# Kernel tuning notes

Hardware: AMD Instinct MI355X
Metric: run time of the kernel (lower is better)

Reference implementation:

```python
import jax, jax.numpy as jnp
import numpy as np

B, S, D, H = 2, 2048, 1024, 16
DH = D // H  # 64


def _rotate_half(t):
    x1, x2 = jnp.split(t, 2, axis=-1)
    return jnp.concatenate([-x2, x1], axis=-1)


def setup_inputs() -> dict:
    key = jax.random.key(0)
    ks = jax.random.split(key, 11)
    x = jax.random.normal(ks[0], (B, S, D), dtype=jnp.float32)
    mask = jax.random.randint(ks[1], (B, S), 0, 2, dtype=jnp.int32)
    scale = 0.02
    wq = jax.random.normal(ks[2], (D, D), dtype=jnp.float32) * scale
    bq = jnp.zeros((D,), dtype=jnp.float32)
    wk = jax.random.normal(ks[3], (D, D), dtype=jnp.float32) * scale
    bk = jnp.zeros((D,), dtype=jnp.float32)
    wv = jax.random.normal(ks[4], (D, D), dtype=jnp.float32) * scale
    bv = jnp.zeros((D,), dtype=jnp.float32)
    wo = jax.random.normal(ks[5], (D, D), dtype=jnp.float32) * scale
    bo = jnp.zeros((D,), dtype=jnp.float32)
    return {"x": x, "mask": mask, "wq": wq, "bq": bq, "wk": wk, "bk": bk,
            "wv": wv, "bv": bv, "wo": wo, "bo": bo}


def reference(x, mask, wq, bq, wk, bk, wv, bv, wo, bo):
    b, s, d = x.shape
    # QKV projections, split heads -> [B, H, S, DH]
    q = (x @ wq + bq).reshape(b, s, H, DH).transpose(0, 2, 1, 3)
    k = (x @ wk + bk).reshape(b, s, H, DH).transpose(0, 2, 1, 3)
    v = (x @ wv + bv).reshape(b, s, H, DH).transpose(0, 2, 1, 3)
    # RoPE exactly as in source: repeat(cos,2) paired with half-split rotate
    pos = jnp.arange(s, dtype=jnp.float32)
    inv_freq = 1.0 / (10000.0 ** (jnp.arange(0, DH, 2, dtype=jnp.float32) / DH))
    angle = pos[:, None] * inv_freq[None, :]            # [S, DH/2]
    cos = jnp.repeat(jnp.cos(angle), 2, axis=-1)[None, None]  # [1,1,S,DH]
    sin = jnp.repeat(jnp.sin(angle), 2, axis=-1)[None, None]
    q = q * cos + _rotate_half(q) * sin
    k = k * cos + _rotate_half(k) * sin
    # scaled dot-product attention with additive mask
    logits = jnp.einsum('bhqd,bhkd->bhqk', q, k) / jnp.sqrt(jnp.float32(DH))
    m = mask.astype(jnp.float32)[:, None, None, :]      # [B,1,1,S]
    logits = logits + m * (-1e9)
    attn = jax.nn.softmax(logits, axis=-1)
    out = jnp.einsum('bhqk,bhkd->bhqd', attn, v)
    out = out.transpose(0, 2, 1, 3).reshape(b, s, d)
    return out @ wo + bo
```

## Files before the change

### kernel.cpp

```cpp
#include <hip/hip_runtime.h>
#include <math.h>

#define BB 2
#define SS 2048
#define DD 1024
#define HH 16

typedef unsigned short u16;
using bf16x8 = __attribute__((ext_vector_type(8))) short;
using f32x4  = __attribute__((ext_vector_type(4))) float;


__device__ __forceinline__ u16 f2bf(float f) {
    unsigned u = __float_as_uint(f);
    unsigned r = u + 0x7fffu + ((u >> 16) & 1u);
    return (u16)(r >> 16);
}

__device__ __forceinline__ void gload_lds16(const void* g, const void* l) {
    __builtin_amdgcn_global_load_lds(
        (const __attribute__((address_space(1))) unsigned int*)(unsigned long long)g,
        (__attribute__((address_space(3))) unsigned int*)(unsigned int)(unsigned long long)l,
        16, 0, 0);
}

__global__ void rope_table(float* __restrict__ cost, float* __restrict__ sint) {
    int idx = blockIdx.x * 256 + threadIdx.x;
    int pos = idx >> 5;
    int j   = idx & 31;
    double inv = pow(10000.0, -(double)j / 32.0);
    double ang = (double)pos * inv;
    cost[idx] = (float)cos(ang);
    sint[idx] = (float)sin(ang);
}

__global__ void cvt_x(const float* __restrict__ x, u16* __restrict__ xb) {
    int i = (blockIdx.x * 256 + threadIdx.x) * 4;
    float4 v = *(const float4*)(x + i);
    ushort4 o;
    o.x = f2bf(v.x); o.y = f2bf(v.y); o.z = f2bf(v.z); o.w = f2bf(v.w);
    *(ushort4*)(xb + i) = o;
}

__global__ void transpose_w(const float* __restrict__ w0, const float* __restrict__ w1,
                            const float* __restrict__ w2, const float* __restrict__ w3,
                            u16* __restrict__ o0, u16* __restrict__ o1,
                            u16* __restrict__ o2, u16* __restrict__ o3) {
    const float* in = (blockIdx.z == 0) ? w0 : (blockIdx.z == 1) ? w1 : (blockIdx.z == 2) ? w2 : w3;
    u16* out        = (blockIdx.z == 0) ? o0 : (blockIdx.z == 1) ? o1 : (blockIdx.z == 2) ? o2 : o3;
    __shared__ float t[32][33];
    int n = blockIdx.x * 32 + threadIdx.x;
    for (int i = threadIdx.y; i < 32; i += 8)
        t[i][threadIdx.x] = in[(size_t)(blockIdx.y * 32 + i) * 1024 + n];
    __syncthreads();
    int k = blockIdx.y * 32 + threadIdx.x;
    for (int i = threadIdx.y; i < 32; i += 8)
        out[(size_t)(blockIdx.x * 32 + i) * 1024 + k] = f2bf(t[threadIdx.x][i]);
}

__global__ __launch_bounds__(256)
void qkv_gemm(const u16* __restrict__ xb,
              const u16* __restrict__ wtq, const u16* __restrict__ wtk, const u16* __restrict__ wtv,
              const float* __restrict__ bq, const float* __restrict__ bk, const float* __restrict__ bv,
              const float* __restrict__ cost, const float* __restrict__ sint,
              u16* __restrict__ qo, u16* __restrict__ ko, u16* __restrict__ vo)
{
    __shared__ u16 Al[128 * 32];
    __shared__ u16 Bl[128 * 32];

    int bx = blockIdx.x;
    int which = bx >> 3;
    int n0 = (bx & 7) << 7;
    int m0 = blockIdx.y << 7;
    const u16*  wt    = (which == 0) ? wtq : (which == 1) ? wtk : wtv;
    const float* bias = (which == 0) ? bq  : (which == 1) ? bk  : bv;

    int t = threadIdx.x;
    int wid = t >> 6, lane = t & 63;
    int wr = wid >> 1, wc = wid & 1;
    int fr = lane & 15, fq = lane >> 4;

    f32x4 acc[4][4];
    #pragma unroll
    for (int m = 0; m < 4; ++m)
        #pragma unroll
        for (int n = 0; n < 4; ++n)
            #pragma unroll
            for (int r = 0; r < 4; ++r) acc[m][n][r] = 0.f;

    int srow = (lane >> 2);
    int skof = (lane & 3) << 3;

    for (int k0 = 0; k0 < 1024; k0 += 32) {
        __syncthreads();
        #pragma unroll
        for (int c = 0; c < 2; ++c) {
            int chunk = wid * 2 + c;
            int row = (chunk << 4) + srow;
            gload_lds16(xb + (size_t)(m0 + row) * 1024 + k0 + skof, &Al[chunk << 9]);
            gload_lds16(wt + (size_t)(n0 + row) * 1024 + k0 + skof, &Bl[chunk << 9]);
        }
        __syncthreads();

        bf16x8 af[4], bf[4];
        #pragma unroll
        for (int m = 0; m < 4; ++m)
            af[m] = *(const bf16x8*)&Al[((wr << 6) + (m << 4) + fr) * 32 + (fq << 3)];
        #pragma unroll
        for (int n = 0; n < 4; ++n)
            bf[n] = *(const bf16x8*)&Bl[((wc << 6) + (n << 4) + fr) * 32 + (fq << 3)];
        #pragma unroll
        for (int m = 0; m < 4; ++m)
            #pragma unroll
            for (int n = 0; n < 4; ++n)
                acc[m][n] = __builtin_amdgcn_mfma_f32_16x16x32_bf16(af[m], bf[n], acc[m][n], 0, 0, 0);
    }

    if (which < 2) {
        u16* outp = (which == 0) ? qo : ko;
        const float qs = (which == 0) ? 0.125f : 1.0f;
        #pragma unroll
        for (int n = 0; n < 2; ++n) {
            int col = n0 + (wc << 6) + (n << 4) + fr;
            int h = col >> 6;
            int d = col & 63;
            float b1 = bias[col], b2 = bias[col + 32];
            int a1 = d >> 1;
            #pragma unroll
            for (int mm = 0; mm < 4; ++mm) {
                #pragma unroll
                for (int j = 0; j < 4; ++j) {
                    int mi = m0 + (wr << 6) + (mm << 4) + (fq << 2) + j;
                    int bi = mi >> 11, s = mi & 2047;
                    float c1 = cost[s * 32 + a1],      s1 = sint[s * 32 + a1];
                    float c2 = cost[s * 32 + a1 + 16], s2 = sint[s * 32 + a1 + 16];
                    float x1 = acc[mm][n][j]     + b1;
                    float x2 = acc[mm][n + 2][j] + b2;
                    size_t base = ((size_t)(bi * HH + h) * SS + s) << 6;
                    outp[base + d]      = f2bf((x1 * c1 - x2 * s1) * qs);
                    outp[base + d + 32] = f2bf((x2 * c2 + x1 * s2) * qs);
                }
            }
        }
    } else {
        #pragma unroll
        for (int n = 0; n < 4; ++n) {
            int col = n0 + (wc << 6) + (n << 4) + fr;
            int h = col >> 6, d = col & 63;
            float bb = bias[col];
            #pragma unroll
            for (int mm = 0; mm < 4; ++mm) {
                #pragma unroll
                for (int j = 0; j < 4; ++j) {
                    int mi = m0 + (wr << 6) + (mm << 4) + (fq << 2) + j;
                    int bi = mi >> 11, s = mi & 2047;
                    vo[((((size_t)(bi * HH + h)) << 6) + d) * SS + s] = f2bf(acc[mm][n][j] + bb);
                }
            }
        }
    }
}

__global__ __launch_bounds__(256, 4)
void attn(const u16* __restrict__ qb, const u16* __restrict__ kb, const u16* __restrict__ vt,
          const int* __restrict__ mask, u16* __restrict__ preb)
{
    __shared__ u16 Kl[2][4096];
    __shared__ u16 Vl[2][4096];
    __shared__ u16 Pl[4][1024];

    const int qb0 = blockIdx.x << 6;
    const int bh  = blockIdx.y;
    const int b   = bh >> 4;
    const int t   = threadIdx.x;
    const int w   = t >> 6;
    const int lane = t & 63;
    const int fr  = lane & 15;
    const int fq  = lane >> 4;
    const int swz = (fr & 7) << 4;

    const char* kbase = (const char*)(kb + ((size_t)bh << 17));
    const char* vbase = (const char*)(vt + ((size_t)bh << 17));
    const int* maskp  = mask + (b << 11);

    const int sbo = ((t & 7) << 4) ^ (((t >> 3) & 7) << 4);

    const int qrow = qb0 + (w << 4) + fr;
    const u16* qp = qb + (((size_t)bh << 11) + qrow) * 64 + (fq << 3);
    bf16x8 qf0 = *(const bf16x8*)qp;
    bf16x8 qf1 = *(const bf16x8*)(qp + 32);

    f32x4 o[4];
    #pragma unroll
    for (int n = 0; n < 4; ++n)
        #pragma unroll
        for (int r = 0; r < 4; ++r) o[n][r] = 0.f;
    float mrun = -INFINITY, lrun = 0.f;

    auto STAGE = [&](int buf, int kt) {
        #pragma unroll
        for (int c = 0; c < 2; ++c) {
            int row = (c << 5) + (t >> 3);
            gload_lds16(kbase + ((size_t)(kt << 6) + row) * 128 + sbo,
                        (const char*)&Kl[buf][0] + (c << 12) + t * 16);
            gload_lds16(vbase + (size_t)row * 4096 + (kt << 7) + sbo,
                        (const char*)&Vl[buf][0] + (c << 12) + t * 16);
        }
    };

    STAGE(0, 0);
    __syncthreads();

    for (int kt = 0; kt < 32; ++kt) {
        const int cur = kt & 1;

        float mb[16];
        #pragma unroll
        for (int g = 0; g < 4; ++g)
            #pragma unroll
            for (int j = 0; j < 4; ++j)
                mb[(g << 2) + j] = -1e9f * (float)maskp[(kt << 6) + (g << 4) + (fq << 2) + j];

        if (kt < 31) STAGE(cur ^ 1, kt + 1);

        f32x4 sv[4];
        #pragma unroll
        for (int g = 0; g < 4; ++g)
            #pragma unroll
            for (int r = 0; r < 4; ++r) sv[g][r] = 0.f;

        const char* Kb = (const char*)&Kl[cur][0];
        #pragma unroll
        for (int g = 0; g < 4; ++g) {
            int row = (g << 4) + fr;
            bf16x8 kf0 = *(const bf16x8*)(Kb + row * 128 + ((fq << 4) ^ swz));
            bf16x8 kf1 = *(const bf16x8*)(Kb + row * 128 + (((fq << 4) + 64) ^ swz));
            sv[g] = __builtin_amdgcn_mfma_f32_16x16x32_bf16(kf0, qf0, sv[g], 0, 0, 0);
            sv[g] = __builtin_amdgcn_mfma_f32_16x16x32_bf16(kf1, qf1, sv[g], 0, 0, 0);
        }

        float tm = -INFINITY;
        #pragma unroll
        for (int g = 0; g < 4; ++g)
            #pragma unroll
            for (int j = 0; j < 4; ++j) {
                sv[g][j] += mb[(g << 2) + j];
                tm = fmaxf(tm, sv[g][j]);
            }
        tm = fmaxf(tm, __shfl_xor(tm, 16));
        tm = fmaxf(tm, __shfl_xor(tm, 32));
        float newm = fmaxf(mrun, tm);
        float scale = __expf(mrun - newm);
        float ps = 0.f;
        #pragma unroll
        for (int g = 0; g < 4; ++g) {
            float p0 = __expf(sv[g][0] - newm);
            float p1 = __expf(sv[g][1] - newm);
            float p2 = __expf(sv[g][2] - newm);
            float p3 = __expf(sv[g][3] - newm);
            ps += (p0 + p1) + (p2 + p3);
            ushort4 pw;
            pw.x = f2bf(p0); pw.y = f2bf(p1); pw.z = f2bf(p2); pw.w = f2bf(p3);
            *(ushort4*)((char*)&Pl[w][0] + fr * 128 + (((g << 5) + (fq << 3)) ^ swz)) = pw;
        }
        ps += __shfl_xor(ps, 16);
        ps += __shfl_xor(ps, 32);
        lrun = lrun * scale + ps;
        mrun = newm;

        #pragma unroll
        for (int j = 0; j < 4; ++j) {
            float sj = __shfl(scale, (lane & 48) + (fq << 2) + j);
            #pragma unroll
            for (int n = 0; n < 4; ++n) o[n][j] *= sj;
        }

        #pragma unroll
        for (int kk = 0; kk < 2; ++kk) {
            bf16x8 pa = *(const bf16x8*)((const char*)&Pl[w][0] + fr * 128 + (((fq << 4) + (kk << 6)) ^ swz));
            #pragma unroll
            for (int n = 0; n < 4; ++n) {
                int row = (n << 4) + fr;
                bf16x8 vf = *(const bf16x8*)((const char*)&Vl[cur][0] + row * 128 + (((fq << 4) + (kk << 6)) ^ swz));
                o[n] = __builtin_amdgcn_mfma_f32_16x16x32_bf16(pa, vf, o[n], 0, 0, 0);
            }
        }
        __syncthreads();
    }

    #pragma unroll
    for (int j = 0; j < 4; ++j) {
        float lj = __shfl(lrun, (lane & 48) + (fq << 2) + j);
        float inv = 1.0f / lj;
        int qr = qb0 + (w << 4) + (fq << 2) + j;
        u16* op = preb + ((size_t)((b << 11) + qr) << 10) + ((bh & 15) << 6) + fr;
        #pragma unroll
        for (int n = 0; n < 4; ++n)
            op[n << 4] = f2bf(o[n][j] * inv);
    }
}

__global__ __launch_bounds__(256)
void out_gemm(const u16* __restrict__ pre, const u16* __restrict__ wto,
              const float* __restrict__ bo, float* __restrict__ outp)
{
    __shared__ u16 Al[128 * 32];
    __shared__ u16 Bl[128 * 32];

    int n0 = blockIdx.x << 7;
    int m0 = blockIdx.y << 7;

    int t = threadIdx.x;
    int wid = t >> 6, lane = t & 63;
    int wr = wid >> 1, wc = wid & 1;
    int fr = lane & 15, fq = lane >> 4;

    f32x4 acc[4][4];
    #pragma unroll
    for (int m = 0; m < 4; ++m)
        #pragma unroll
        for (int n = 0; n < 4; ++n)
            #pragma unroll
            for (int r = 0; r < 4; ++r) acc[m][n][r] = 0.f;

    int srow = (lane >> 2);
    int skof = (lane & 3) << 3;

    for (int k0 = 0; k0 < 1024; k0 += 32) {
        __syncthreads();
        #pragma unroll
        for (int c = 0; c < 2; ++c) {
            int chunk = wid * 2 + c;
            int row = (chunk << 4) + srow;
            gload_lds16(pre + (size_t)(m0 + row) * 1024 + k0 + skof, &Al[chunk << 9]);
            gload_lds16(wto + (size_t)(n0 + row) * 1024 + k0 + skof, &Bl[chunk << 9]);
        }
        __syncthreads();

        bf16x8 af[4], bf[4];
        #pragma unroll
        for (int m = 0; m < 4; ++m)
            af[m] = *(const bf16x8*)&Al[((wr << 6) + (m << 4) + fr) * 32 + (fq << 3)];
        #pragma unroll
        for (int n = 0; n < 4; ++n)
            bf[n] = *(const bf16x8*)&Bl[((wc << 6) + (n << 4) + fr) * 32 + (fq << 3)];
        #pragma unroll
        for (int m = 0; m < 4; ++m)
            #pragma unroll
            for (int n = 0; n < 4; ++n)
                acc[m][n] = __builtin_amdgcn_mfma_f32_16x16x32_bf16(af[m], bf[n], acc[m][n], 0, 0, 0);
    }

    #pragma unroll
    for (int n = 0; n < 4; ++n) {
        int col = n0 + (wc << 6) + (n << 4) + fr;
        float bb = bo[col];
        #pragma unroll
        for (int m = 0; m < 4; ++m) {
            #pragma unroll
            for (int j = 0; j < 4; ++j) {
                int mi = m0 + (wr << 6) + (m << 4) + (fq << 2) + j;
                outp[(size_t)mi * 1024 + col] = acc[m][n][j] + bb;
            }
        }
    }
}

extern "C" void kernel_launch(void* const* d_in, const int* in_sizes, int n_in,
                              void* d_out, int out_size, void* d_ws, size_t ws_size,
                              hipStream_t stream) {
    const float* x    = (const float*)d_in[0];
    const int*   mask = (const int*)  d_in[1];
    const float* wq   = (const float*)d_in[2];
    const float* bq   = (const float*)d_in[3];
    const float* wk   = (const float*)d_in[4];
    const float* bk   = (const float*)d_in[5];
    const float* wv   = (const float*)d_in[6];
    const float* bv   = (const float*)d_in[7];
    const float* wo   = (const float*)d_in[8];
    const float* bo   = (const float*)d_in[9];
    float* out = (float*)d_out;
    float* ws  = (float*)d_ws;

    float* cosT = ws;
    float* sinT = ws + 65536;
    u16* xb    = (u16*)(ws + 131072);
    u16* wtq   = xb    + 4194304;
    u16* wtk   = wtq   + 1048576;
    u16* wtv   = wtk   + 1048576;
    u16* wto   = wtv   + 1048576;
    u16* qbuf  = wto   + 1048576;
    u16* kbuf  = qbuf  + 4194304;
    u16* vtbuf = kbuf  + 4194304;
    u16* preb  = vtbuf + 4194304;

    hipLaunchKernelGGL(rope_table, dim3(256), dim3(256), 0, stream, cosT, sinT);
    hipLaunchKernelGGL(cvt_x, dim3(4096), dim3(256), 0, stream, x, xb);
    hipLaunchKernelGGL(transpose_w, dim3(32, 32, 4), dim3(32, 8), 0, stream,
                       wq, wk, wv, wo, wtq, wtk, wtv, wto);
    hipLaunchKernelGGL(qkv_gemm, dim3(24, 32), dim3(256), 0, stream,
                       xb, wtq, wtk, wtv, bq, bk, bv, cosT, sinT, qbuf, kbuf, vtbuf);
    hipLaunchKernelGGL(attn, dim3(32, 32), dim3(256), 0, stream,
                       qbuf, kbuf, vtbuf, mask, preb);
    hipLaunchKernelGGL(out_gemm, dim3(8, 32), dim3(256), 0, stream, preb, wto, bo, out);
}
```

Before: 240.4 us.

## Rework attention softmax, V layout, mask bias, RoPE tables and block scheduling

Several changes land together. The softmax moves to the exp2 domain, with log2e folded into the Q scale and the mask bias, and the O/l rescale is skipped whenever the running max grows by 11 or less. Probabilities are packed with v_cvt_pk_bf16_f32, and the MFMA sections get s_setprio raised. V is now written row-major from the GEMM with coalesced stores and transposed by a separate kernel instead of scattered strided stores. The RoPE tables are transposed so the epilogue can read them as float4, the mask is precomputed as a float bias, and attention blocks are remapped so that each XCD handles the same heads for L2 locality. The costs are an extra kernel launch plus a round trip through the V buffer, and the deferred rescale relies on a lazy-max bound staying within fp32 range.

```diff
diff --git a/kernel.cpp b/kernel.cpp
--- a/kernel.cpp
+++ b/kernel.cpp
@@ -9,6 +9,8 @@
 typedef unsigned short u16;
 using bf16x8 = __attribute__((ext_vector_type(8))) short;
 using f32x4  = __attribute__((ext_vector_type(4))) float;
+
+#define LOG2E 1.44269504f
 
 
 __device__ __forceinline__ u16 f2bf(float f) {
@@ -26,12 +28,17 @@
 
 __global__ void rope_table(float* __restrict__ cost, float* __restrict__ sint) {
     int idx = blockIdx.x * 256 + threadIdx.x;
-    int pos = idx >> 5;
-    int j   = idx & 31;
+    int j   = idx >> 11;
+    int pos = idx & 2047;
     double inv = pow(10000.0, -(double)j / 32.0);
     double ang = (double)pos * inv;
     cost[idx] = (float)cos(ang);
     sint[idx] = (float)sin(ang);
+}
+
+__global__ void mkbias(const int* __restrict__ mask, float* __restrict__ mb) {
+    int i = blockIdx.x * 256 + threadIdx.x;
+    mb[i] = -1.44269504e9f * (float)mask[i];
 }
 
 __global__ void cvt_x(const float* __restrict__ x, u16* __restrict__ xb) {
@@ -118,7 +125,7 @@
 
     if (which < 2) {
         u16* outp = (which == 0) ? qo : ko;
-        const float qs = (which == 0) ? 0.125f : 1.0f;
+        const float qs = (which == 0) ? 0.125f * LOG2E : 1.0f;
         #pragma unroll
         for (int n = 0; n < 2; ++n) {
             int col = n0 + (wc << 6) + (n << 4) + fr;
@@ -128,17 +135,23 @@
             int a1 = d >> 1;
             #pragma unroll
             for (int mm = 0; mm < 4; ++mm) {
+                int mi0 = m0 + (wr << 6) + (mm << 4) + (fq << 2);
+                int bi = mi0 >> 11, s0 = mi0 & 2047;
+                float4 c1 = *(const float4*)(cost + (a1 << 11) + s0);
+                float4 s1 = *(const float4*)(sint + (a1 << 11) + s0);
+                float4 c2 = *(const float4*)(cost + ((a1 + 16) << 11) + s0);
+                float4 s2 = *(const float4*)(sint + ((a1 + 16) << 11) + s0);
+                const float* c1p = (const float*)&c1;
+                const float* s1p = (const float*)&s1;
+                const float* c2p = (const float*)&c2;
+                const float* s2p = (const float*)&s2;
                 #pragma unroll
                 for (int j = 0; j < 4; ++j) {
-                    int mi = m0 + (wr << 6) + (mm << 4) + (fq << 2) + j;
-                    int bi = mi >> 11, s = mi & 2047;
-                    float c1 = cost[s * 32 + a1],      s1 = sint[s * 32 + a1];
-                    float c2 = cost[s * 32 + a1 + 16], s2 = sint[s * 32 + a1 + 16];
                     float x1 = acc[mm][n][j]     + b1;
                     float x2 = acc[mm][n + 2][j] + b2;
-                    size_t base = ((size_t)(bi * HH + h) * SS + s) << 6;
-                    outp[base + d]      = f2bf((x1 * c1 - x2 * s1) * qs);
-                    outp[base + d + 32] = f2bf((x2 * c2 + x1 * s2) * qs);
+                    size_t base = ((size_t)(bi * HH + h) * SS + s0 + j) << 6;
+                    outp[base + d]      = f2bf((x1 * c1p[j] - x2 * s1p[j]) * qs);
+                    outp[base + d + 32] = f2bf((x2 * c2p[j] + x1 * s2p[j]) * qs);
                 }
             }
         }
@@ -154,23 +167,45 @@
                 for (int j = 0; j < 4; ++j) {
                     int mi = m0 + (wr << 6) + (mm << 4) + (fq << 2) + j;
                     int bi = mi >> 11, s = mi & 2047;
-                    vo[((((size_t)(bi * HH + h)) << 6) + d) * SS + s] = f2bf(acc[mm][n][j] + bb);
+                    vo[(((size_t)(bi * HH + h) * SS + s) << 6) + d] = f2bf(acc[mm][n][j] + bb);
                 }
             }
         }
     }
 }
 
+__global__ __launch_bounds__(256)
+void transpose_v(const u16* __restrict__ vin, u16* __restrict__ vout) {
+    __shared__ u16 Ld[64][72];
+    int stile = blockIdx.x;
+    int bh    = blockIdx.y;
+    int t = threadIdx.x;
+    int r = t >> 2, seg = (t & 3) << 4;
+    const u16* src = vin + (((size_t)bh * SS + (stile << 6) + r) << 6) + seg;
+    *(uint4*)&Ld[r][seg]     = *(const uint4*)src;
+    *(uint4*)&Ld[r][seg + 8] = *(const uint4*)(src + 8);
+    __syncthreads();
+    u16 tmp[16];
+    #pragma unroll
+    for (int i = 0; i < 16; ++i) tmp[i] = Ld[seg + i][r];
+    u16* dst = vout + ((size_t)(bh << 6) + r) * SS + (stile << 6) + seg;
+    *(uint4*)dst       = *(const uint4*)&tmp[0];
+    *(uint4*)(dst + 8) = *(const uint4*)&tmp[8];
+}
+
 __global__ __launch_bounds__(256, 4)
 void attn(const u16* __restrict__ qb, const u16* __restrict__ kb, const u16* __restrict__ vt,
-          const int* __restrict__ mask, u16* __restrict__ preb)
+          const float* __restrict__ mbias, u16* __restrict__ preb)
 {
     __shared__ u16 Kl[2][4096];
     __shared__ u16 Vl[2][4096];
     __shared__ u16 Pl[4][1024];
 
-    const int qb0 = blockIdx.x << 6;
-    const int bh  = blockIdx.y;
+    const int bid = blockIdx.x;
+    const int xcd = bid & 7;
+    const int idx = bid >> 3;
+    const int bh  = (xcd << 2) | (idx >> 5);
+    const int qb0 = (idx & 31) << 6;
     const int b   = bh >> 4;
     const int t   = threadIdx.x;
     const int w   = t >> 6;
@@ -181,7 +216,7 @@
 
     const char* kbase = (const char*)(kb + ((size_t)bh << 17));
     const char* vbase = (const char*)(vt + ((size_t)bh << 17));
-    const int* maskp  = mask + (b << 11);
+    const float* mbp  = mbias + (b << 11);
 
     const int sbo = ((t & 7) << 4) ^ (((t >> 3) & 7) << 4);
 
@@ -214,22 +249,16 @@
     for (int kt = 0; kt < 32; ++kt) {
         const int cur = kt & 1;
 
-        float mb[16];
+        if (kt < 31) STAGE(cur ^ 1, kt + 1);
+
+        f32x4 sv[4];
         #pragma unroll
         for (int g = 0; g < 4; ++g)
             #pragma unroll
-            for (int j = 0; j < 4; ++j)
-                mb[(g << 2) + j] = -1e9f * (float)maskp[(kt << 6) + (g << 4) + (fq << 2) + j];
-
-        if (kt < 31) STAGE(cur ^ 1, kt + 1);
-
-        f32x4 sv[4];
-        #pragma unroll
-        for (int g = 0; g < 4; ++g)
-            #pragma unroll
             for (int r = 0; r < 4; ++r) sv[g][r] = 0.f;
 
         const char* Kb = (const char*)&Kl[cur][0];
+        __builtin_amdgcn_s_setprio(1);
         #pragma unroll
         for (int g = 0; g < 4; ++g) {
             int row = (g << 4) + fr;
@@ -238,43 +267,50 @@
             sv[g] = __builtin_amdgcn_mfma_f32_16x16x32_bf16(kf0, qf0, sv[g], 0, 0, 0);
             sv[g] = __builtin_amdgcn_mfma_f32_16x16x32_bf16(kf1, qf1, sv[g], 0, 0, 0);
         }
+        __builtin_amdgcn_s_setprio(0);
 
         float tm = -INFINITY;
         #pragma unroll
-        for (int g = 0; g < 4; ++g)
-            #pragma unroll
-            for (int j = 0; j < 4; ++j) {
-                sv[g][j] += mb[(g << 2) + j];
-                tm = fmaxf(tm, sv[g][j]);
-            }
+        for (int g = 0; g < 4; ++g) {
+            const float4 m4 = *(const float4*)(mbp + (kt << 6) + (g << 4) + (fq << 2));
+            sv[g][0] += m4.x; sv[g][1] += m4.y; sv[g][2] += m4.z; sv[g][3] += m4.w;
+            tm = fmaxf(tm, fmaxf(fmaxf(sv[g][0], sv[g][1]), fmaxf(sv[g][2], sv[g][3])));
+        }
         tm = fmaxf(tm, __shfl_xor(tm, 16));
         tm = fmaxf(tm, __shfl_xor(tm, 32));
-        float newm = fmaxf(mrun, tm);
-        float scale = __expf(mrun - newm);
+
+        if (!__all(tm <= mrun + 11.0f)) {
+            float newm = fmaxf(mrun, tm);
+            float scale = __builtin_amdgcn_exp2f(mrun - newm);
+            lrun *= scale;
+            #pragma unroll
+            for (int j = 0; j < 4; ++j) {
+                float sj = __shfl(scale, (lane & 48) + (fq << 2) + j);
+                #pragma unroll
+                for (int n = 0; n < 4; ++n) o[n][j] *= sj;
+            }
+            mrun = newm;
+        }
+
         float ps = 0.f;
         #pragma unroll
         for (int g = 0; g < 4; ++g) {
-            float p0 = __expf(sv[g][0] - newm);
-            float p1 = __expf(sv[g][1] - newm);
-            float p2 = __expf(sv[g][2] - newm);
-            float p3 = __expf(sv[g][3] - newm);
+            float p0 = __builtin_amdgcn_exp2f(sv[g][0] - mrun);
+            float p1 = __builtin_amdgcn_exp2f(sv[g][1] - mrun);
+            float p2 = __builtin_amdgcn_exp2f(sv[g][2] - mrun);
+            float p3 = __builtin_amdgcn_exp2f(sv[g][3] - mrun);
             ps += (p0 + p1) + (p2 + p3);
-            ushort4 pw;
-            pw.x = f2bf(p0); pw.y = f2bf(p1); pw.z = f2bf(p2); pw.w = f2bf(p3);
-            *(ushort4*)((char*)&Pl[w][0] + fr * 128 + (((g << 5) + (fq << 3)) ^ swz)) = pw;
+            unsigned r0, r1;
+            asm("v_cvt_pk_bf16_f32 %0, %1, %2" : "=v"(r0) : "v"(p0), "v"(p1));
+            asm("v_cvt_pk_bf16_f32 %0, %1, %2" : "=v"(r1) : "v"(p2), "v"(p3));
+            uint2 pw; pw.x = r0; pw.y = r1;
+            *(uint2*)((char*)&Pl[w][0] + fr * 128 + (((g << 5) + (fq << 3)) ^ swz)) = pw;
         }
         ps += __shfl_xor(ps, 16);
         ps += __shfl_xor(ps, 32);
-        lrun = lrun * scale + ps;
-        mrun = newm;
-
-        #pragma unroll
-        for (int j = 0; j < 4; ++j) {
-            float sj = __shfl(scale, (lane & 48) + (fq << 2) + j);
-            #pragma unroll
-            for (int n = 0; n < 4; ++n) o[n][j] *= sj;
-        }
-
+        lrun += ps;
+
+        __builtin_amdgcn_s_setprio(1);
         #pragma unroll
         for (int kk = 0; kk < 2; ++kk) {
             bf16x8 pa = *(const bf16x8*)((const char*)&Pl[w][0] + fr * 128 + (((fq << 4) + (kk << 6)) ^ swz));
@@ -285,6 +321,7 @@
                 o[n] = __builtin_amdgcn_mfma_f32_16x16x32_bf16(pa, vf, o[n], 0, 0, 0);
             }
         }
+        __builtin_amdgcn_s_setprio(0);
         __syncthreads();
     }
 
@@ -382,25 +419,29 @@
     float* out = (float*)d_out;
     float* ws  = (float*)d_ws;
 
-    float* cosT = ws;
-    float* sinT = ws + 65536;
-    u16* xb    = (u16*)(ws + 131072);
+    float* cosT  = ws;
+    float* sinT  = ws + 65536;
+    float* mbias = ws + 131072;
+    u16* xb    = (u16*)(ws + 135168);
     u16* wtq   = xb    + 4194304;
     u16* wtk   = wtq   + 1048576;
     u16* wtv   = wtk   + 1048576;
     u16* wto   = wtv   + 1048576;
     u16* qbuf  = wto   + 1048576;
     u16* kbuf  = qbuf  + 4194304;
-    u16* vtbuf = kbuf  + 4194304;
-    u16* preb  = vtbuf + 4194304;
+    u16* vbuf  = kbuf  + 4194304;
+    u16* preb  = vbuf  + 4194304;
+    u16* vtbuf = xb;
 
     hipLaunchKernelGGL(rope_table, dim3(256), dim3(256), 0, stream, cosT, sinT);
+    hipLaunchKernelGGL(mkbias, dim3(16), dim3(256), 0, stream, mask, mbias);
     hipLaunchKernelGGL(cvt_x, dim3(4096), dim3(256), 0, stream, x, xb);
     hipLaunchKernelGGL(transpose_w, dim3(32, 32, 4), dim3(32, 8), 0, stream,
                        wq, wk, wv, wo, wtq, wtk, wtv, wto);
     hipLaunchKernelGGL(qkv_gemm, dim3(24, 32), dim3(256), 0, stream,
-                       xb, wtq, wtk, wtv, bq, bk, bv, cosT, sinT, qbuf, kbuf, vtbuf);
-    hipLaunchKernelGGL(attn, dim3(32, 32), dim3(256), 0, stream,
-                       qbuf, kbuf, vtbuf, mask, preb);
+                       xb, wtq, wtk, wtv, bq, bk, bv, cosT, sinT, qbuf, kbuf, vbuf);
+    hipLaunchKernelGGL(transpose_v, dim3(32, 32), dim3(256), 0, stream, vbuf, vtbuf);
+    hipLaunchKernelGGL(attn, dim3(1024), dim3(256), 0, stream,
+                       qbuf, kbuf, vtbuf, mbias, preb);
     hipLaunchKernelGGL(out_gemm, dim3(8, 32), dim3(256), 0, stream, preb, wto, bo, out);
 }
```

Result: no change. 241.4 us (+0.4%).
